# Kernel optimization log

Hardware: AMD Instinct MI355X
Metric: run time of the kernel (lower is better)

## Reference

```python
import jax, jax.numpy as jnp
import numpy as np

S, B, E, H, M = 1024, 4, 1024, 16, 128  # seq, batch, embed, heads, model_dims (key width)
V = E // H                              # value_dims = 64
_WSCALE = 1.0 / np.sqrt(E)              # keep softmax logits O(1)


def _cplx(re, im):
    return jax.lax.complex(re, im)


def setup_inputs() -> dict:
    key = jax.random.key(0)
    ks = jax.random.split(key, 10)
    n = lambda k, shp: jax.random.normal(k, shp, dtype=jnp.float32)
    w = lambda k, shp: n(k, shp) * np.float32(_WSCALE / np.sqrt(2.0))
    return {
        "logits_re": n(ks[0], (S, B, E)),
        "logits_im": n(ks[1], (S, B, E)),
        "wq_re": w(ks[2], (H, M, E)), "wq_im": w(ks[3], (H, M, E)),
        "wk_re": w(ks[4], (H, M, E)), "wk_im": w(ks[5], (H, M, E)),
        "wv_re": w(ks[6], (H, V, E)), "wv_im": w(ks[7], (H, V, E)),
        "wo_re": w(ks[8], (E, E)),    "wo_im": w(ks[9], (E, E)),
    }


def reference(logits_re, logits_im, wq_re, wq_im, wk_re, wk_im,
              wv_re, wv_im, wo_re, wo_im):
    x = _cplx(logits_re, logits_im)          # (s, b, e) complex64
    wq = _cplx(wq_re, wq_im)                 # (h, m, e)
    wk = _cplx(wk_re, wk_im)
    wv = _cplx(wv_re, wv_im)                 # (h, v, e)
    wo = _cplx(wo_re, wo_im)                 # (e, e)

    q = jnp.einsum('hme,sbe->bhsm', wq, x)   # (b, h, s, m)
    k = jnp.einsum('hme,sbe->bhsm', wk, x)
    v = jnp.einsum('hve,sbe->bhsv', wv, x)   # (b, h, s, v)

    scores = jnp.einsum('bhsm,bhtm->bhst', q, k)         # complex, no conjugation (matches torch matmul)
    amp = jnp.abs(scores)                                # -> float32
    causal = jnp.triu(jnp.ones((S, S), dtype=bool), 1)   # True above diagonal -> masked
    amp = jnp.where(causal, -jnp.inf, amp) / jnp.sqrt(jnp.float32(M))
    attn = jax.nn.softmax(amp, axis=-1).astype(scores.dtype)  # cast back to complex64

    upd = jnp.einsum('bhst,bhtv->bhsv', attn, v)         # (b, h, s, v)
    upd = upd.transpose(2, 0, 1, 3).reshape(S, B, E)     # 's2 b (h v)'
    out = jnp.einsum('sbe,ef->sbf', upd, wo) + x         # residual
    # complex output returned as stacked (real, imag) float32 for harness compatibility
    return jnp.stack([out.real, out.imag])
```

## Files before the change

### kernel.cpp

```cpp
#include <hip/hip_runtime.h>
#include <math.h>

#define S_DIM 1024
#define B_DIM 4
#define E_DIM 1024
#define H_DIM 16
#define M_DIM 128
#define V_DIM 64

typedef __attribute__((ext_vector_type(8))) short short8;
typedef __attribute__((ext_vector_type(4))) float f32x4;
typedef __attribute__((ext_vector_type(4))) int int4v;

__device__ __forceinline__ unsigned short f2bf(float f) {
    union { float f; unsigned u; } v; v.f = f;
    unsigned r = v.u + 0x7FFFu + ((v.u >> 16) & 1u);
    return (unsigned short)(r >> 16);
}

__device__ __forceinline__ void async16(const unsigned short* g, unsigned short* l) {
    __builtin_amdgcn_global_load_lds(
        (const __attribute__((address_space(1))) void*)g,
        (__attribute__((address_space(3))) void*)l,
        16, 0, 0);
}

__global__ __launch_bounds__(256) void convert_pair(
    const float* __restrict__ re, const float* __restrict__ im,
    unsigned short* __restrict__ dre, unsigned short* __restrict__ dim_, int n4)
{
    int i = blockIdx.x * 256 + threadIdx.x;
    if (i >= n4) return;
    float4 r = ((const float4*)re)[i];
    float4 m = ((const float4*)im)[i];
    ushort4 ro, mo;
    ro.x = f2bf(r.x); ro.y = f2bf(r.y); ro.z = f2bf(r.z); ro.w = f2bf(r.w);
    mo.x = f2bf(m.x); mo.y = f2bf(m.y); mo.z = f2bf(m.z); mo.w = f2bf(m.w);
    ((ushort4*)dre)[i] = ro;
    ((ushort4*)dim_)[i] = mo;
}

__global__ __launch_bounds__(256) void transpose_wo(
    const float* __restrict__ wore, const float* __restrict__ woim,
    unsigned short* __restrict__ wtre, unsigned short* __restrict__ wtim)
{
    __shared__ float tr[32][33], ti[32][33];
    const int bx = blockIdx.x * 32;
    const int by = blockIdx.y * 32;
    const int tx = threadIdx.x & 31, ty = threadIdx.x >> 5;
    for (int i = ty; i < 32; i += 8) {
        tr[i][tx] = wore[(bx + i) * E_DIM + by + tx];
        ti[i][tx] = woim[(bx + i) * E_DIM + by + tx];
    }
    __syncthreads();
    for (int i = ty; i < 32; i += 8) {
        wtre[(by + i) * E_DIM + bx + tx] = f2bf(tr[tx][i]);
        wtim[(by + i) * E_DIM + bx + tx] = f2bf(ti[tx][i]);
    }
}

__global__ __launch_bounds__(256) void vtrans(
    const unsigned short* __restrict__ vrp, const unsigned short* __restrict__ vip,
    unsigned short* __restrict__ vrt, unsigned short* __restrict__ vit)
{
    __shared__ unsigned short tl[2][64][66];
    const int tid = threadIdx.x;
    const int t0 = blockIdx.x * 64;
    const int bh = blockIdx.y;
    #pragma unroll
    for (int pl = 0; pl < 2; ++pl) {
        const unsigned short* src = pl ? vip : vrp;
        #pragma unroll
        for (int p = 0; p < 2; ++p) {
            const int row = p * 32 + (tid >> 3);
            const int col = (tid & 7) * 8;
            short8 d = *(const short8*)&src[((size_t)bh * S_DIM + t0 + row) * V_DIM + col];
            #pragma unroll
            for (int j = 0; j < 8; ++j) tl[pl][row][col + j] = (unsigned short)d[j];
        }
    }
    __syncthreads();
    #pragma unroll
    for (int pl = 0; pl < 2; ++pl) {
        unsigned short* dst = pl ? vit : vrt;
        #pragma unroll
        for (int p = 0; p < 2; ++p) {
            const int v = p * 32 + (tid >> 3);
            const int tc = (tid & 7) * 8;
            short8 d;
            #pragma unroll
            for (int j = 0; j < 8; ++j) d[j] = (short)tl[pl][tc + j][v];
            *(short8*)&dst[((size_t)bh * V_DIM + v) * S_DIM + t0 + tc] = d;
        }
    }
}

template<int MODE>
__global__ __launch_bounds__(256, 3) void cgemm(
    const unsigned short* __restrict__ Are, const unsigned short* __restrict__ Aim,
    const unsigned short* __restrict__ Bre, const unsigned short* __restrict__ Bim,
    unsigned short* __restrict__ qrp, unsigned short* __restrict__ qip,
    unsigned short* __restrict__ krp, unsigned short* __restrict__ kip,
    unsigned short* __restrict__ vrp, unsigned short* __restrict__ vip,
    const float* __restrict__ xre, const float* __restrict__ xim,
    float* __restrict__ out)
{
    __shared__ unsigned short lds[24576];
    const int tid  = threadIdx.x;
    const int wave = tid >> 6;
    const int lane = tid & 63;
    const int r0 = blockIdx.x * 128;
    const int j0 = blockIdx.y * 64;
    const int wm = (wave >> 1) * 64;
    const int wn = (wave & 1) * 32;

    f32x4 accre[4][2], accim[4][2];
    #pragma unroll
    for (int i = 0; i < 4; ++i)
        #pragma unroll
        for (int j = 0; j < 2; ++j) {
            accre[i][j] = (f32x4){0.f, 0.f, 0.f, 0.f};
            accim[i][j] = (f32x4){0.f, 0.f, 0.f, 0.f};
        }

    const int srow = lane >> 2;
    const int scol = (lane & 3) * 8;
    const int fr = lane & 15;
    const int fk = (lane >> 4) * 8;

    for (int k0 = 0; k0 < E_DIM; k0 += 64) {
        __syncthreads();
        #pragma unroll
        for (int kk = 0; kk < 2; ++kk) {
            const int kb = kk * 12288;
            const int kg = k0 + kk * 32;
            #pragma unroll
            for (int c = 0; c < 2; ++c) {
                const int row0 = wave * 32 + c * 16;
                const int g = (r0 + row0 + srow) * E_DIM + kg + scol;
                async16(Are + g, &lds[kb + row0 * 32]);
                async16(Aim + g, &lds[kb + 4096 + row0 * 32]);
            }
            {
                const int row0 = wave * 16;
                const int g = (j0 + row0 + srow) * E_DIM + kg + scol;
                async16(Bre + g, &lds[kb + 8192 + row0 * 32]);
                async16(Bim + g, &lds[kb + 10240 + row0 * 32]);
            }
        }
        __syncthreads();

        #pragma unroll
        for (int kk = 0; kk < 2; ++kk) {
            const int kb = kk * 12288;
            short8 ar[4], ai[4];
            #pragma unroll
            for (int im = 0; im < 4; ++im) {
                const int row = wm + im * 16 + fr;
                ar[im] = *(const short8*)&lds[kb + row * 32 + fk];
                ai[im] = *(const short8*)&lds[kb + 4096 + row * 32 + fk];
            }
            #pragma unroll
            for (int jn = 0; jn < 2; ++jn) {
                const int row = wn + jn * 16 + fr;
                const short8 br = *(const short8*)&lds[kb + 8192 + row * 32 + fk];
                const short8 bi = *(const short8*)&lds[kb + 10240 + row * 32 + fk];
                int4v t = *(int4v*)&bi;
                t = t ^ (int)0x80008000;
                const short8 bin = *(short8*)&t;
                #pragma unroll
                for (int im = 0; im < 4; ++im) {
                    accre[im][jn] = __builtin_amdgcn_mfma_f32_16x16x32_bf16(ar[im], br,  accre[im][jn], 0, 0, 0);
                    accre[im][jn] = __builtin_amdgcn_mfma_f32_16x16x32_bf16(ai[im], bin, accre[im][jn], 0, 0, 0);
                    accim[im][jn] = __builtin_amdgcn_mfma_f32_16x16x32_bf16(ar[im], bi,  accim[im][jn], 0, 0, 0);
                    accim[im][jn] = __builtin_amdgcn_mfma_f32_16x16x32_bf16(ai[im], br,  accim[im][jn], 0, 0, 0);
                }
            }
        }
    }

    #pragma unroll
    for (int im = 0; im < 4; ++im) {
        #pragma unroll
        for (int reg = 0; reg < 4; ++reg) {
            const int r = r0 + wm + im * 16 + (lane >> 4) * 4 + reg;
            #pragma unroll
            for (int jn = 0; jn < 2; ++jn) {
                const int j = j0 + wn + jn * 16 + fr;
                const float vr = accre[im][jn][reg];
                const float vi = accim[im][jn][reg];
                if (MODE == 0) {
                    const int s = r >> 2, b = r & 3;
                    if (j < 2048) {
                        const int h = j >> 7, m = j & 127;
                        const size_t off = ((size_t)(b * H_DIM + h) * S_DIM + s) * M_DIM + m;
                        qrp[off] = f2bf(vr); qip[off] = f2bf(vi);
                    } else if (j < 4096) {
                        const int jl = j - 2048, h = jl >> 7, m = jl & 127;
                        const size_t off = ((size_t)(b * H_DIM + h) * S_DIM + s) * M_DIM + m;
                        krp[off] = f2bf(vr); kip[off] = f2bf(vi);
                    } else {
                        const int jl = j - 4096, h = jl >> 6, vv = jl & 63;
                        const size_t off = ((size_t)(b * H_DIM + h) * S_DIM + s) * V_DIM + vv;
                        vrp[off] = f2bf(vr); vip[off] = f2bf(vi);
                    }
                } else {
                    const int idx = r * E_DIM + j;
                    out[idx] = vr + xre[idx];
                    out[S_DIM * B_DIM * E_DIM + idx] = vi + xim[idx];
                }
            }
        }
    }
}

__global__ __launch_bounds__(256, 2) void attn_mfma(
    const unsigned short* __restrict__ qr, const unsigned short* __restrict__ qi,
    const unsigned short* __restrict__ kr, const unsigned short* __restrict__ ki,
    const unsigned short* __restrict__ vrt, const unsigned short* __restrict__ vit,
    unsigned short* __restrict__ updre, unsigned short* __restrict__ updim)
{
    __shared__ __align__(16) unsigned short Ks[2][64][136];
    __shared__ __align__(16) unsigned short Vs[2][64][72];
    __shared__ __align__(16) unsigned short Ps[4][16][80];

    const int tid  = threadIdx.x;
    const int wave = tid >> 6;
    const int lane = tid & 63;
    const int qt = (int)gridDim.x - 1 - blockIdx.x;
    const int bh = blockIdx.y;
    const int q0 = qt * 64;
    const size_t base_qk = (size_t)bh * S_DIM * M_DIM;
    const size_t base_v  = (size_t)bh * V_DIM * S_DIM;

    const int fr = lane & 15;
    const int fg = lane >> 4;
    const int fk = fg * 8;

    const int krow = tid >> 4, kcol = (tid & 15) * 8;
    const int vrow = tid >> 3, vcol = (tid & 7) * 8;

    #pragma unroll
    for (int pl = 0; pl < 2; ++pl) {
        const unsigned short* src = pl ? qi : qr;
        #pragma unroll
        for (int p = 0; p < 4; ++p)
            *(short8*)&Ks[pl][p * 16 + krow][kcol] =
                *(const short8*)&src[base_qk + (size_t)(q0 + p * 16 + krow) * M_DIM + kcol];
    }
    __syncthreads();
    short8 Bqr[4], Bqi[4];
    {
        const int qrow = wave * 16 + fr;
        #pragma unroll
        for (int ks = 0; ks < 4; ++ks) {
            Bqr[ks] = *(const short8*)&Ks[0][qrow][ks * 32 + fk];
            Bqi[ks] = *(const short8*)&Ks[1][qrow][ks * 32 + fk];
        }
    }

    f32x4 Ore[4], Oim[4];
    #pragma unroll
    for (int vt = 0; vt < 4; ++vt) {
        Ore[vt] = (f32x4){0.f, 0.f, 0.f, 0.f};
        Oim[vt] = (f32x4){0.f, 0.f, 0.f, 0.f};
    }
    float mrun = -INFINITY, lrun = 0.f;

    const float scale = 0.088388347648318447f;
    const int qglob = q0 + wave * 16 + fr;

    short8 pk[2][4], pv[2][2];
    #pragma unroll
    for (int pl = 0; pl < 2; ++pl) {
        const unsigned short* src = pl ? ki : kr;
        #pragma unroll
        for (int p = 0; p < 4; ++p)
            pk[pl][p] = *(const short8*)&src[base_qk + (size_t)(p * 16 + krow) * M_DIM + kcol];
    }
    #pragma unroll
    for (int pl = 0; pl < 2; ++pl) {
        const unsigned short* src = pl ? vit : vrt;
        #pragma unroll
        for (int p = 0; p < 2; ++p)
            pv[pl][p] = *(const short8*)&src[base_v + (size_t)(p * 32 + vrow) * S_DIM + vcol];
    }

    for (int t0 = 0; t0 <= q0; t0 += 64) {
        __syncthreads();
        #pragma unroll
        for (int pl = 0; pl < 2; ++pl) {
            #pragma unroll
            for (int p = 0; p < 4; ++p)
                *(short8*)&Ks[pl][p * 16 + krow][kcol] = pk[pl][p];
            #pragma unroll
            for (int p = 0; p < 2; ++p)
                *(short8*)&Vs[pl][p * 32 + vrow][vcol] = pv[pl][p];
        }
        __syncthreads();

        if (t0 + 64 <= q0) {
            const int tn = t0 + 64;
            #pragma unroll
            for (int pl = 0; pl < 2; ++pl) {
                const unsigned short* src = pl ? ki : kr;
                #pragma unroll
                for (int p = 0; p < 4; ++p)
                    pk[pl][p] = *(const short8*)&src[base_qk + (size_t)(tn + p * 16 + krow) * M_DIM + kcol];
            }
            #pragma unroll
            for (int pl = 0; pl < 2; ++pl) {
                const unsigned short* src = pl ? vit : vrt;
                #pragma unroll
                for (int p = 0; p < 2; ++p)
                    pv[pl][p] = *(const short8*)&src[base_v + (size_t)(p * 32 + vrow) * S_DIM + tn + vcol];
            }
        }

        f32x4 Sre[4], Sim[4];
        #pragma unroll
        for (int tt = 0; tt < 4; ++tt) {
            Sre[tt] = (f32x4){0.f, 0.f, 0.f, 0.f};
            Sim[tt] = (f32x4){0.f, 0.f, 0.f, 0.f};
            const int trow = tt * 16 + fr;
            #pragma unroll
            for (int ks = 0; ks < 4; ++ks) {
                const short8 Akr = *(const short8*)&Ks[0][trow][ks * 32 + fk];
                const short8 Aki = *(const short8*)&Ks[1][trow][ks * 32 + fk];
                int4v t = *(int4v*)&Aki;
                t = t ^ (int)0x80008000;
                const short8 Akin = *(short8*)&t;
                Sre[tt] = __builtin_amdgcn_mfma_f32_16x16x32_bf16(Akr,  Bqr[ks], Sre[tt], 0, 0, 0);
                Sre[tt] = __builtin_amdgcn_mfma_f32_16x16x32_bf16(Akin, Bqi[ks], Sre[tt], 0, 0, 0);
                Sim[tt] = __builtin_amdgcn_mfma_f32_16x16x32_bf16(Akr,  Bqi[ks], Sim[tt], 0, 0, 0);
                Sim[tt] = __builtin_amdgcn_mfma_f32_16x16x32_bf16(Aki,  Bqr[ks], Sim[tt], 0, 0, 0);
            }
        }

        float amp[4][4];
        float rowmax = -INFINITY;
        #pragma unroll
        for (int tt = 0; tt < 4; ++tt) {
            #pragma unroll
            for (int r = 0; r < 4; ++r) {
                const int tg = t0 + tt * 16 + fg * 4 + r;
                const float re = Sre[tt][r], im = Sim[tt][r];
                const float a = sqrtf(re * re + im * im) * scale;
                const float av = (tg > qglob) ? -INFINITY : a;
                amp[tt][r] = av;
                rowmax = fmaxf(rowmax, av);
            }
        }
        rowmax = fmaxf(rowmax, __shfl_xor(rowmax, 16));
        rowmax = fmaxf(rowmax, __shfl_xor(rowmax, 32));
        const float nm = fmaxf(mrun, rowmax);
        const float alpha = __expf(mrun - nm);
        mrun = nm;
        float psum = 0.f;
        #pragma unroll
        for (int tt = 0; tt < 4; ++tt) {
            #pragma unroll
            for (int r = 0; r < 4; ++r) {
                const float p = __expf(amp[tt][r] - nm);
                psum += p;
                Ps[wave][fr][tt * 16 + fg * 4 + r] = f2bf(p);
            }
        }
        psum += __shfl_xor(psum, 16);
        psum += __shfl_xor(psum, 32);
        lrun = lrun * alpha + psum;

        #pragma unroll
        for (int vt = 0; vt < 4; ++vt)
            #pragma unroll
            for (int r = 0; r < 4; ++r) { Ore[vt][r] *= alpha; Oim[vt][r] *= alpha; }

        const short8 Bp0 = *(const short8*)&Ps[wave][fr][fk];
        const short8 Bp1 = *(const short8*)&Ps[wave][fr][32 + fk];
        #pragma unroll
        for (int vt = 0; vt < 4; ++vt) {
            const int vr2 = vt * 16 + fr;
            const short8 Ar0 = *(const short8*)&Vs[0][vr2][fk];
            const short8 Ar1 = *(const short8*)&Vs[0][vr2][32 + fk];
            const short8 Ai0 = *(const short8*)&Vs[1][vr2][fk];
            const short8 Ai1 = *(const short8*)&Vs[1][vr2][32 + fk];
            Ore[vt] = __builtin_amdgcn_mfma_f32_16x16x32_bf16(Ar0, Bp0, Ore[vt], 0, 0, 0);
            Ore[vt] = __builtin_amdgcn_mfma_f32_16x16x32_bf16(Ar1, Bp1, Ore[vt], 0, 0, 0);
            Oim[vt] = __builtin_amdgcn_mfma_f32_16x16x32_bf16(Ai0, Bp0, Oim[vt], 0, 0, 0);
            Oim[vt] = __builtin_amdgcn_mfma_f32_16x16x32_bf16(Ai1, Bp1, Oim[vt], 0, 0, 0);
        }
    }

    const int b = bh >> 4, h = bh & 15;
    const float inv = 1.0f / lrun;
    const size_t base = ((size_t)(qglob * B_DIM + b)) * E_DIM + h * V_DIM;
    #pragma unroll
    for (int vt = 0; vt < 4; ++vt) {
        ushort4 pr, pi;
        pr.x = f2bf(Ore[vt][0] * inv); pr.y = f2bf(Ore[vt][1] * inv);
        pr.z = f2bf(Ore[vt][2] * inv); pr.w = f2bf(Ore[vt][3] * inv);
        pi.x = f2bf(Oim[vt][0] * inv); pi.y = f2bf(Oim[vt][1] * inv);
        pi.z = f2bf(Oim[vt][2] * inv); pi.w = f2bf(Oim[vt][3] * inv);
        *(ushort4*)&updre[base + vt * 16 + fg * 4] = pr;
        *(ushort4*)&updim[base + vt * 16 + fg * 4] = pi;
    }
}

extern "C" void kernel_launch(void* const* d_in, const int* in_sizes, int n_in,
                              void* d_out, int out_size, void* d_ws, size_t ws_size,
                              hipStream_t stream) {
    const float* xre  = (const float*)d_in[0];
    const float* xim  = (const float*)d_in[1];
    const float* wqre = (const float*)d_in[2];
    const float* wqim = (const float*)d_in[3];
    const float* wkre = (const float*)d_in[4];
    const float* wkim = (const float*)d_in[5];
    const float* wvre = (const float*)d_in[6];
    const float* wvim = (const float*)d_in[7];
    const float* wore = (const float*)d_in[8];
    const float* woim = (const float*)d_in[9];
    float* out = (float*)d_out;

    char* p = (char*)d_ws;
    const size_t QK = (size_t)B_DIM * H_DIM * S_DIM * M_DIM;
    const size_t VS = (size_t)B_DIM * H_DIM * S_DIM * V_DIM;
    const size_t SBE = (size_t)S_DIM * B_DIM * E_DIM;
    unsigned short* qrw = (unsigned short*)p;  p += QK * 2;
    unsigned short* qiw = (unsigned short*)p;  p += QK * 2;
    unsigned short* krw = (unsigned short*)p;  p += QK * 2;
    unsigned short* kiw = (unsigned short*)p;  p += QK * 2;
    unsigned short* vrw = (unsigned short*)p;  p += VS * 2;
    unsigned short* viw = (unsigned short*)p;  p += VS * 2;
    unsigned short* vrt = (unsigned short*)p;  p += VS * 2;
    unsigned short* vit = (unsigned short*)p;  p += VS * 2;
    unsigned short* updre = (unsigned short*)p; p += SBE * 2;
    unsigned short* updim = (unsigned short*)p; p += SBE * 2;
    unsigned short* xbre  = (unsigned short*)p; p += SBE * 2;
    unsigned short* xbim  = (unsigned short*)p; p += SBE * 2;
    unsigned short* wbre  = (unsigned short*)p; p += (size_t)5120 * E_DIM * 2;
    unsigned short* wbim  = (unsigned short*)p; p += (size_t)5120 * E_DIM * 2;
    unsigned short* wtre  = (unsigned short*)p; p += (size_t)E_DIM * E_DIM * 2;
    unsigned short* wtim  = (unsigned short*)p; p += (size_t)E_DIM * E_DIM * 2;

    convert_pair<<<4096, 256, 0, stream>>>(xre, xim, xbre, xbim, 1048576);
    convert_pair<<<2048, 256, 0, stream>>>(wqre, wqim, wbre, wbim, 524288);
    convert_pair<<<2048, 256, 0, stream>>>(wkre, wkim, wbre + 2048*1024, wbim + 2048*1024, 524288);
    convert_pair<<<1024, 256, 0, stream>>>(wvre, wvim, wbre + 4096*1024, wbim + 4096*1024, 262144);
    transpose_wo<<<dim3(32, 32), 256, 0, stream>>>(wore, woim, wtre, wtim);

    cgemm<0><<<dim3(32, 80), 256, 0, stream>>>(xbre, xbim, wbre, wbim,
                                               qrw, qiw, krw, kiw, vrw, viw,
                                               nullptr, nullptr, nullptr);
    vtrans<<<dim3(16, 64), 256, 0, stream>>>(vrw, viw, vrt, vit);
    attn_mfma<<<dim3(16, 64), 256, 0, stream>>>(qrw, qiw, krw, kiw, vrt, vit, updre, updim);
    cgemm<1><<<dim3(32, 16), 256, 0, stream>>>(updre, updim, wtre, wtim,
                                               nullptr, nullptr, nullptr, nullptr, nullptr, nullptr,
                                               xre, xim, out);
}
```

Measured before the change: 496.5 us.

## Rewrite complex GEMM with 128x128 tiles, 4-stage async LDS pipeline and swizzle

The complex GEMM kernel now uses 512-thread blocks computing 128x128 output tiles instead of 256 threads on 128x64. Operand loads go through a 4-deep ring of LDS buffers with explicit vmcnt waits, so global-to-LDS copies for later k-slices overlap the MFMA work on the current slice. An XOR swizzle on LDS columns aims to reduce bank conflicts, and s_setprio raises priority during the MFMA phase. The cost is 128KB of LDS per block and fewer blocks per CU, and the hand-placed waitcnt/barrier ordering is fragile.

```diff
diff --git a/kernel.cpp b/kernel.cpp
--- a/kernel.cpp
+++ b/kernel.cpp
@@ -96,7 +96,7 @@
 }
 
 template<int MODE>
-__global__ __launch_bounds__(256, 3) void cgemm(
+__global__ __launch_bounds__(512, 2) void cgemm(
     const unsigned short* __restrict__ Are, const unsigned short* __restrict__ Aim,
     const unsigned short* __restrict__ Bre, const unsigned short* __restrict__ Bim,
     unsigned short* __restrict__ qrp, unsigned short* __restrict__ qip,
@@ -105,14 +105,14 @@
     const float* __restrict__ xre, const float* __restrict__ xim,
     float* __restrict__ out)
 {
-    __shared__ unsigned short lds[24576];
+    __shared__ __align__(16) unsigned short lds[65536];
     const int tid  = threadIdx.x;
     const int wave = tid >> 6;
     const int lane = tid & 63;
     const int r0 = blockIdx.x * 128;
-    const int j0 = blockIdx.y * 64;
-    const int wm = (wave >> 1) * 64;
-    const int wn = (wave & 1) * 32;
+    const int j0 = blockIdx.y * 128;
+    const int wm = (wave >> 2) * 64;
+    const int wn = (wave & 3) * 32;
 
     f32x4 accre[4][2], accim[4][2];
     #pragma unroll
@@ -123,61 +123,68 @@
             accim[i][j] = (f32x4){0.f, 0.f, 0.f, 0.f};
         }
 
-    const int srow = lane >> 2;
-    const int scol = (lane & 3) * 8;
     const int fr = lane & 15;
-    const int fk = (lane >> 4) * 8;
-
-    for (int k0 = 0; k0 < E_DIM; k0 += 64) {
-        __syncthreads();
-        #pragma unroll
-        for (int kk = 0; kk < 2; ++kk) {
-            const int kb = kk * 12288;
-            const int kg = k0 + kk * 32;
-            #pragma unroll
-            for (int c = 0; c < 2; ++c) {
-                const int row0 = wave * 32 + c * 16;
-                const int g = (r0 + row0 + srow) * E_DIM + kg + scol;
-                async16(Are + g, &lds[kb + row0 * 32]);
-                async16(Aim + g, &lds[kb + 4096 + row0 * 32]);
-            }
-            {
-                const int row0 = wave * 16;
-                const int g = (j0 + row0 + srow) * E_DIM + kg + scol;
-                async16(Bre + g, &lds[kb + 8192 + row0 * 32]);
-                async16(Bim + g, &lds[kb + 10240 + row0 * 32]);
-            }
-        }
-        __syncthreads();
-
-        #pragma unroll
-        for (int kk = 0; kk < 2; ++kk) {
-            const int kb = kk * 12288;
-            short8 ar[4], ai[4];
+    const int xc = ((lane >> 4) ^ ((lane >> 1) & 3)) * 8;
+
+    const int srow = tid >> 2;
+    const int scol = ((tid & 3) ^ ((tid >> 3) & 3)) * 8;
+
+    #define STAGE(sl) { \
+        const int col_ = (sl) * 32 + scol; \
+        unsigned short* d_ = &lds[(((sl) & 3) << 14) + tid * 8]; \
+        async16(Are + (size_t)(r0 + srow) * E_DIM + col_, d_); \
+        async16(Aim + (size_t)(r0 + srow) * E_DIM + col_, d_ + 4096); \
+        async16(Bre + (size_t)(j0 + srow) * E_DIM + col_, d_ + 8192); \
+        async16(Bim + (size_t)(j0 + srow) * E_DIM + col_, d_ + 12288); }
+
+    STAGE(0) STAGE(1) STAGE(2)
+    asm volatile("s_waitcnt vmcnt(8)" ::: "memory");
+    __builtin_amdgcn_s_barrier();
+
+    #pragma unroll 1
+    for (int s = 0; s < 32; ++s) {
+        if (s < 29) STAGE(s + 3)
+
+        const unsigned short* buf = &lds[(s & 3) << 14];
+        short8 ar[4], ai[4], brr[2], bii[2];
+        #pragma unroll
+        for (int im = 0; im < 4; ++im) {
+            const int ro = (wm + im * 16 + fr) * 32 + xc;
+            ar[im] = *(const short8*)&buf[ro];
+            ai[im] = *(const short8*)&buf[4096 + ro];
+        }
+        #pragma unroll
+        for (int jn = 0; jn < 2; ++jn) {
+            const int ro = (wn + jn * 16 + fr) * 32 + xc;
+            brr[jn] = *(const short8*)&buf[8192 + ro];
+            bii[jn] = *(const short8*)&buf[12288 + ro];
+        }
+
+        if (s < 29)       { asm volatile("s_waitcnt vmcnt(8)" ::: "memory"); }
+        else if (s == 29) { asm volatile("s_waitcnt vmcnt(4)" ::: "memory"); }
+        else              { asm volatile("s_waitcnt vmcnt(0)" ::: "memory"); }
+        __builtin_amdgcn_s_barrier();
+        asm volatile("s_waitcnt lgkmcnt(0)" ::: "memory");
+        __builtin_amdgcn_sched_barrier(0);
+
+        __builtin_amdgcn_s_setprio(1);
+        #pragma unroll
+        for (int jn = 0; jn < 2; ++jn) {
+            int4v t = *(int4v*)&bii[jn];
+            t = t ^ (int)0x80008000;
+            const short8 bin = *(short8*)&t;
             #pragma unroll
             for (int im = 0; im < 4; ++im) {
-                const int row = wm + im * 16 + fr;
-                ar[im] = *(const short8*)&lds[kb + row * 32 + fk];
-                ai[im] = *(const short8*)&lds[kb + 4096 + row * 32 + fk];
-            }
-            #pragma unroll
-            for (int jn = 0; jn < 2; ++jn) {
-                const int row = wn + jn * 16 + fr;
-                const short8 br = *(const short8*)&lds[kb + 8192 + row * 32 + fk];
-                const short8 bi = *(const short8*)&lds[kb + 10240 + row * 32 + fk];
-                int4v t = *(int4v*)&bi;
-                t = t ^ (int)0x80008000;
-                const short8 bin = *(short8*)&t;
-                #pragma unroll
-                for (int im = 0; im < 4; ++im) {
-                    accre[im][jn] = __builtin_amdgcn_mfma_f32_16x16x32_bf16(ar[im], br,  accre[im][jn], 0, 0, 0);
-                    accre[im][jn] = __builtin_amdgcn_mfma_f32_16x16x32_bf16(ai[im], bin, accre[im][jn], 0, 0, 0);
-                    accim[im][jn] = __builtin_amdgcn_mfma_f32_16x16x32_bf16(ar[im], bi,  accim[im][jn], 0, 0, 0);
-                    accim[im][jn] = __builtin_amdgcn_mfma_f32_16x16x32_bf16(ai[im], br,  accim[im][jn], 0, 0, 0);
-                }
-            }
-        }
-    }
+                accre[im][jn] = __builtin_amdgcn_mfma_f32_16x16x32_bf16(ar[im], brr[jn], accre[im][jn], 0, 0, 0);
+                accre[im][jn] = __builtin_amdgcn_mfma_f32_16x16x32_bf16(ai[im], bin,     accre[im][jn], 0, 0, 0);
+                accim[im][jn] = __builtin_amdgcn_mfma_f32_16x16x32_bf16(ar[im], bii[jn], accim[im][jn], 0, 0, 0);
+                accim[im][jn] = __builtin_amdgcn_mfma_f32_16x16x32_bf16(ai[im], brr[jn], accim[im][jn], 0, 0, 0);
+            }
+        }
+        __builtin_amdgcn_s_setprio(0);
+        __builtin_amdgcn_s_barrier();
+    }
+    #undef STAGE
 
     #pragma unroll
     for (int im = 0; im < 4; ++im) {
@@ -448,12 +455,12 @@
     convert_pair<<<1024, 256, 0, stream>>>(wvre, wvim, wbre + 4096*1024, wbim + 4096*1024, 262144);
     transpose_wo<<<dim3(32, 32), 256, 0, stream>>>(wore, woim, wtre, wtim);
 
-    cgemm<0><<<dim3(32, 80), 256, 0, stream>>>(xbre, xbim, wbre, wbim,
+    cgemm<0><<<dim3(32, 40), 512, 0, stream>>>(xbre, xbim, wbre, wbim,
                                                qrw, qiw, krw, kiw, vrw, viw,
                                                nullptr, nullptr, nullptr);
     vtrans<<<dim3(16, 64), 256, 0, stream>>>(vrw, viw, vrt, vit);
     attn_mfma<<<dim3(16, 64), 256, 0, stream>>>(qrw, qiw, krw, kiw, vrt, vit, updre, updim);
-    cgemm<1><<<dim3(32, 16), 256, 0, stream>>>(updre, updim, wtre, wtim,
-                                               nullptr, nullptr, nullptr, nullptr, nullptr, nullptr,
-                                               xre, xim, out);
-}
+    cgemm<1><<<dim3(32, 8), 512, 0, stream>>>(updre, updim, wtre, wtim,
+                                              nullptr, nullptr, nullptr, nullptr, nullptr, nullptr,
+                                              xre, xim, out);
+}
```

After: 507.7 us. +2.3%, slower.
